# Kernel tuning notes

Hardware: AMD Instinct MI355X
Metric: run time of the kernel (lower is better)

Reference implementation:

```python
import jax, jax.numpy as jnp
import numpy as np

FFT_NORM = 'forward'


def setup_inputs() -> dict:
    key = jax.random.key(0)
    ks = jax.random.split(key, 6)
    B, N, Cin, Cout, T, M = 16, 16384, 64, 64, 256, 2049  # M = modes//2+1 with modes=4096
    x = jax.random.normal(ks[0], (B, N, Cin), dtype=jnp.float32)
    t_emb = jax.random.normal(ks[1], (B, T), dtype=jnp.float32)
    scale = 1.0 / jnp.sqrt(jnp.float32(Cin))
    weights_real = jax.random.normal(ks[2], (M, Cin, Cout), dtype=jnp.float32) * scale
    weights_imag = jax.random.normal(ks[3], (M, Cin, Cout), dtype=jnp.float32) * scale
    dense_real_w = jax.random.normal(ks[4], (M, T), dtype=jnp.float32) * (1.0 / jnp.sqrt(jnp.float32(T)))
    dense_imag_w = jax.random.normal(ks[5], (M, T), dtype=jnp.float32) * (1.0 / jnp.sqrt(jnp.float32(T)))
    return {"x": x, "t_emb": t_emb, "weights_real": weights_real,
            "weights_imag": weights_imag, "dense_real_w": dense_real_w,
            "dense_imag_w": dense_imag_w}


def reference(x, t_emb, weights_real, weights_imag, dense_real_w, dense_imag_w):
    B, N, _ = x.shape
    M, _, Cout = weights_real.shape  # M = modes//2+1
    W = weights_real + 1j * weights_imag  # (M, Cin, Cout) complex64
    # FFT along the grid axis
    x_ft = jnp.fft.rfft(x, axis=-2, norm=FFT_NORM)  # (B, N//2+1, Cin) complex64
    # Time modulation: eqx Linear (bias-free) = t_emb @ W^T
    t_mod = (t_emb @ dense_real_w.T) + 1j * (t_emb @ dense_imag_w.T)  # (B, M)
    # Diagonal modulation + channel mix, exactly equal to the eye/einsum pair:
    # out[b,i,o] = t_mod[b,i] * sum_c x_ft[b,i,c] * W[i,c,o]
    out_trunc = jnp.einsum('bi,bic,ico->bio', t_mod, x_ft[:, :M, :], W)  # (B, M, Cout)
    out_ft = jnp.zeros((B, N // 2 + 1, Cout), dtype=jnp.complex64)
    out_ft = out_ft.at[:, :M, :].set(out_trunc)
    out = jnp.fft.irfft(out_ft, axis=-2, n=N, norm=FFT_NORM)  # (B, N, Cout) float32
    return out
```

## Files before the change

kernel.cpp:

```cpp
#include <hip/hip_runtime.h>
#include <math.h>

#define B_   16
#define N_   16384
#define LOGN 14
#define CIN  64
#define COUT 64
#define T_   256
#define M_   2049

__device__ __forceinline__ unsigned br14(unsigned v) {
  return __brev(v) >> 18;
}

__device__ __forceinline__ int SW(int n) {
  return (n & ~31) | ((n ^ (n >> 5) ^ (n >> 10)) & 31);
}

__device__ __forceinline__ void cmul(float ar, float ai, float br, float bi,
                                     float& rr, float& ri) {
  rr = ar * br - ai * bi;
  ri = ar * bi + ai * br;
}

__device__ __constant__ float C16[16] = {
  1.f, 0.92387953251f, 0.70710678119f, 0.38268343236f, 0.f, -0.38268343236f,
  -0.70710678119f, -0.92387953251f, -1.f, -0.92387953251f, -0.70710678119f,
  -0.38268343236f, 0.f, 0.38268343236f, 0.70710678119f, 0.92387953251f};
__device__ __constant__ float S16[16] = {
  0.f, 0.38268343236f, 0.70710678119f, 0.92387953251f, 1.f, 0.92387953251f,
  0.70710678119f, 0.38268343236f, 0.f, -0.38268343236f, -0.70710678119f,
  -0.92387953251f, -1.f, -0.92387953251f, -0.70710678119f, -0.38268343236f};

template <int SIGN, int S0>
__device__ __forceinline__ void group16(float* __restrict__ sre,
                                        float* __restrict__ sim, int tid) {
  const int lo = tid & ((1 << S0) - 1);
  const int hi = tid >> S0;
  const int base = (hi << (S0 + 4)) + lo;
  int pp[16];
  float xr[16], xi[16];
#pragma unroll
  for (int j = 0; j < 16; ++j) {
    pp[j] = SW(base + (j << S0));
    xr[j] = sre[pp[j]];
    xi[j] = sim[pp[j]];
  }
  float th = 6.283185307179586f * (float)lo / (float)(16 << S0);
  float sn, cs;
  __sincosf(th, &sn, &cs);
  float w1r = cs, w1i = (float)SIGN * sn;
  float w2r, w2i, w4r, w4i, w8r, w8i;
  cmul(w1r, w1i, w1r, w1i, w2r, w2i);
  cmul(w2r, w2i, w2r, w2i, w4r, w4i);
  cmul(w4r, w4i, w4r, w4i, w8r, w8i);
  {
#pragma unroll
    for (int j = 0; j < 16; j += 2) {
      float br, bi;
      cmul(xr[j + 1], xi[j + 1], w8r, w8i, br, bi);
      xr[j + 1] = xr[j] - br; xi[j + 1] = xi[j] - bi;
      xr[j] += br; xi[j] += bi;
    }
  }
  {
    float tr[2], ti[2];
    tr[0] = w4r; ti[0] = w4i;
    cmul(w4r, w4i, C16[4], (float)SIGN * S16[4], tr[1], ti[1]);
#pragma unroll
    for (int j = 0; j < 16; ++j) {
      if ((j & 2) == 0) {
        int jl = j & 1;
        float br, bi;
        cmul(xr[j + 2], xi[j + 2], tr[jl], ti[jl], br, bi);
        xr[j + 2] = xr[j] - br; xi[j + 2] = xi[j] - bi;
        xr[j] += br; xi[j] += bi;
      }
    }
  }
  {
    float tr[4], ti[4];
#pragma unroll
    for (int jl = 0; jl < 4; ++jl)
      cmul(w2r, w2i, C16[2 * jl], (float)SIGN * S16[2 * jl], tr[jl], ti[jl]);
#pragma unroll
    for (int j = 0; j < 16; ++j) {
      if ((j & 4) == 0) {
        int jl = j & 3;
        float br, bi;
        cmul(xr[j + 4], xi[j + 4], tr[jl], ti[jl], br, bi);
        xr[j + 4] = xr[j] - br; xi[j + 4] = xi[j] - bi;
        xr[j] += br; xi[j] += bi;
      }
    }
  }
  {
    float tr[8], ti[8];
#pragma unroll
    for (int jl = 0; jl < 8; ++jl)
      cmul(w1r, w1i, C16[jl], (float)SIGN * S16[jl], tr[jl], ti[jl]);
#pragma unroll
    for (int j = 0; j < 8; ++j) {
      float br, bi;
      cmul(xr[j + 8], xi[j + 8], tr[j], ti[j], br, bi);
      xr[j + 8] = xr[j] - br; xi[j + 8] = xi[j] - bi;
      xr[j] += br; xi[j] += bi;
    }
  }
#pragma unroll
  for (int j = 0; j < 16; ++j) {
    sre[pp[j]] = xr[j];
    sim[pp[j]] = xi[j];
  }
}

template <int SIGN>
__device__ __forceinline__ void stage12(float* __restrict__ sre,
                                        float* __restrict__ sim, int tid) {
  const int lo0 = tid & 511;
  const int gg  = tid >> 9;
  float th = 6.283185307179586f * (float)lo0 / 8192.0f;
  float sn, cs;
  __sincosf(th, &sn, &cs);
  float wtr = cs, wti = (float)SIGN * sn;
#pragma unroll
  for (int s = 0; s < 8; ++s) {
    float twr, twi;
    cmul(wtr, wti, C16[s], (float)SIGN * S16[s], twr, twi);
    int lo = lo0 + 512 * s;
    int i0 = (gg << 13) + lo;
    int p0 = SW(i0), p1 = SW(i0 + 4096);
    float br, bi;
    cmul(sre[p1], sim[p1], twr, twi, br, bi);
    float ar = sre[p0], ai = sim[p0];
    sre[p0] = ar + br; sim[p0] = ai + bi;
    sre[p1] = ar - br; sim[p1] = ai - bi;
  }
}

template <int SIGN>
__device__ __forceinline__ void stage13(float* __restrict__ sre,
                                        float* __restrict__ sim, int tid) {
  float th = 6.283185307179586f * (float)tid / 16384.0f;
  float sn, cs;
  __sincosf(th, &sn, &cs);
  float wtr = cs, wti = (float)SIGN * sn;
#pragma unroll
  for (int s = 0; s < 8; ++s) {
    float twr, twi;
    cmul(wtr, wti, C16[s], (float)SIGN * S16[s], twr, twi);
    int i0 = tid + 1024 * s;
    int p0 = SW(i0), p1 = SW(i0 + 8192);
    float br, bi;
    cmul(sre[p1], sim[p1], twr, twi, br, bi);
    float ar = sre[p0], ai = sim[p0];
    sre[p0] = ar + br; sim[p0] = ai + bi;
    sre[p1] = ar - br; sim[p1] = ai - bi;
  }
}

__device__ __forceinline__ void decode_bc(int id, int& b, int& cp) {
  int q = id >> 6, r = (id >> 3) & 7, p = id & 7;
  int g = q * 8 + p;
  b  = g >> 2;
  cp = (g & 3) * 8 + r;
}

__global__ __launch_bounds__(256) void tmod_kernel(
    const float* __restrict__ t_emb,
    const float* __restrict__ dwr, const float* __restrict__ dwi,
    float* __restrict__ tmr, float* __restrict__ tmi) {
  int wave = threadIdx.x >> 6;
  int lane = threadIdx.x & 63;
  int p = blockIdx.x * 4 + wave;
  if (p >= B_ * M_) return;
  int b = p / M_, i = p % M_;
  float ar = 0.f, ai = 0.f;
  for (int j = 0; j < 4; ++j) {
    int t = lane + 64 * j;
    float te = t_emb[b * T_ + t];
    ar += te * dwr[(size_t)i * T_ + t];
    ai += te * dwi[(size_t)i * T_ + t];
  }
  for (int off = 32; off > 0; off >>= 1) {
    ar += __shfl_down(ar, off, 64);
    ai += __shfl_down(ai, off, 64);
  }
  if (lane == 0) { tmr[b * M_ + i] = ar; tmi[b * M_ + i] = ai; }
}

__global__ __launch_bounds__(1024) void fft_fwd_fused(
    const float* __restrict__ x,
    float* __restrict__ Xre, float* __restrict__ Xim) {
  __shared__ float sre[N_], sim[N_];
  int b, cp;
  decode_bc(blockIdx.x, b, cp);
  const int tid = threadIdx.x;
  const float* xb = x + (size_t)b * N_ * CIN + 2 * cp;
  float2 v[16];
#pragma unroll
  for (int s = 0; s < 16; ++s) {
    int n = tid + 1024 * s;
    v[s] = *(const float2*)(xb + (size_t)n * CIN);
  }
#pragma unroll
  for (int s = 0; s < 16; ++s) {
    int n = tid + 1024 * s;
    int rr = SW((int)br14((unsigned)n));
    sre[rr] = v[s].x;
    sim[rr] = v[s].y;
  }
  __syncthreads();
  group16<-1, 0>(sre, sim, tid); __syncthreads();
  group16<-1, 4>(sre, sim, tid); __syncthreads();
  group16<-1, 8>(sre, sim, tid); __syncthreads();
  stage12<-1>(sre, sim, tid);    __syncthreads();
  stage13<-1>(sre, sim, tid);    __syncthreads();
  const float sc = 1.0f / (float)N_;
  size_t o0 = (size_t)(b * CIN + 2 * cp) * M_;
  size_t o1 = o0 + M_;
  for (int k = tid; k < M_; k += 1024) {
    int mk = (N_ - k) & (N_ - 1);
    int pk = SW(k), pm = SW(mk);
    float zr = sre[pk], zi = sim[pk];
    float mr = sre[pm], mi = sim[pm];
    float X0r = 0.5f * (zr + mr), X0i = 0.5f * (zi - mi);
    float X1r = 0.5f * (zi + mi), X1i = -0.5f * (zr - mr);
    Xre[o0 + k] = X0r * sc; Xim[o0 + k] = X0i * sc;
    Xre[o1 + k] = X1r * sc; Xim[o1 + k] = X1i * sc;
  }
}

__global__ __launch_bounds__(256) void transpose2(
    const float* __restrict__ s0, const float* __restrict__ s1,
    float* __restrict__ d0, float* __restrict__ d1, int R, int C) {
  __shared__ float tile[32][33];
  const float* src = blockIdx.z ? s1 : s0;
  float* dst = blockIdx.z ? d1 : d0;
  int c0 = blockIdx.x * 32, r0 = blockIdx.y * 32;
  int tx = threadIdx.x & 31, ty = threadIdx.x >> 5;
  for (int p = 0; p < 32; p += 8) {
    int r = r0 + ty + p, c = c0 + tx;
    tile[ty + p][tx] = (r < R && c < C) ? src[(size_t)r * C + c] : 0.f;
  }
  __syncthreads();
  for (int p = 0; p < 32; p += 8) {
    int r = c0 + ty + p, c = r0 + tx;
    if (r < C && c < R) dst[(size_t)r * R + c] = tile[tx][ty + p];
  }
}

typedef short  s8v  __attribute__((ext_vector_type(8)));
typedef float  f4v  __attribute__((ext_vector_type(4)));

__device__ __forceinline__ unsigned short f2bf_hi(float x) {
  unsigned u = __float_as_uint(x);
  unsigned r = (u + 0x7fffu + ((u >> 16) & 1u)) >> 16;
  return (unsigned short)r;
}

__device__ __forceinline__ int fbi(int k, int n) {
  return ((((n >> 4) * 2 + (k >> 5)) << 9) | (((n & 15) + (((k >> 3) & 3) << 4)) << 3) | (k & 7));
}
__device__ __forceinline__ int fai(int k, int m) {
  return (((k >> 5) << 9) | (((m & 15) + (((k >> 3) & 3) << 4)) << 3) | (k & 7));
}

__global__ __launch_bounds__(256) void mix_mfma(
    const float* __restrict__ Xtr, const float* __restrict__ Xti,
    const float* __restrict__ Wr_g, const float* __restrict__ Wi_g,
    const float* __restrict__ tmr, const float* __restrict__ tmi,
    float* __restrict__ Yr_g, float* __restrict__ Yi_g) {
  __shared__ __align__(16) unsigned short BrH[4096], BrL[4096], BiH[4096], BiL[4096];
  __shared__ __align__(16) unsigned short ArH[1024], ArL[1024];
  __shared__ __align__(16) unsigned short AiH[1024], AiL[1024];
  __shared__ __align__(16) unsigned short AnH[1024], AnL[1024];
  __shared__ float tms[32];
  const int i   = blockIdx.x;
  const int tid = threadIdx.x;

  const float4* wr4 = (const float4*)(Wr_g + (size_t)i * 4096);
  const float4* wi4 = (const float4*)(Wi_g + (size_t)i * 4096);
#pragma unroll
  for (int it = 0; it < 4; ++it) {
    int f4 = it * 256 + tid;
    float4 vr = wr4[f4];
    float4 vi = wi4[f4];
    int idx0 = f4 * 4;
    float er[4] = {vr.x, vr.y, vr.z, vr.w};
    float ei[4] = {vi.x, vi.y, vi.z, vi.w};
#pragma unroll
    for (int e = 0; e < 4; ++e) {
      int idx = idx0 + e;
      int k = idx >> 6, n = idx & 63;
      int a = fbi(k, n);
      unsigned short h = f2bf_hi(er[e]);
      float hf = __uint_as_float(((unsigned)h) << 16);
      BrH[a] = h; BrL[a] = f2bf_hi(er[e] - hf);
      h = f2bf_hi(ei[e]);
      hf = __uint_as_float(((unsigned)h) << 16);
      BiH[a] = h; BiL[a] = f2bf_hi(ei[e] - hf);
    }
  }
  {
    float4 vr = ((const float4*)(Xtr + (size_t)i * 1024))[tid];
    float4 vi = ((const float4*)(Xti + (size_t)i * 1024))[tid];
    float er[4] = {vr.x, vr.y, vr.z, vr.w};
    float ei[4] = {vi.x, vi.y, vi.z, vi.w};
    int idx0 = tid * 4;
#pragma unroll
    for (int e = 0; e < 4; ++e) {
      int idx = idx0 + e;
      int m = idx >> 6, k = idx & 63;
      int a = fai(k, m);
      unsigned short h = f2bf_hi(er[e]);
      float hf = __uint_as_float(((unsigned)h) << 16);
      ArH[a] = h; ArL[a] = f2bf_hi(er[e] - hf);
      h = f2bf_hi(ei[e]);
      hf = __uint_as_float(((unsigned)h) << 16);
      unsigned short l = f2bf_hi(ei[e] - __uint_as_float(((unsigned)h) << 16));
      AiH[a] = h; AiL[a] = l;
      AnH[a] = h ^ 0x8000u; AnL[a] = l ^ 0x8000u;
    }
  }
  if (tid < 16) {
    tms[tid]      = tmr[tid * M_ + i];
    tms[16 + tid] = tmi[tid * M_ + i];
  }
  __syncthreads();

  const int w = tid >> 6, L = tid & 63;
  const s8v* pArH = (const s8v*)ArH; const s8v* pArL = (const s8v*)ArL;
  const s8v* pAiH = (const s8v*)AiH; const s8v* pAiL = (const s8v*)AiL;
  const s8v* pAnH = (const s8v*)AnH; const s8v* pAnL = (const s8v*)AnL;
  const s8v* pBrH = (const s8v*)BrH; const s8v* pBrL = (const s8v*)BrL;
  const s8v* pBiH = (const s8v*)BiH; const s8v* pBiL = (const s8v*)BiL;

  f4v cr = {0.f, 0.f, 0.f, 0.f}, ci = {0.f, 0.f, 0.f, 0.f};
#pragma unroll
  for (int s = 0; s < 2; ++s) {
    s8v arh = pArH[s * 64 + L], arl = pArL[s * 64 + L];
    s8v aih = pAiH[s * 64 + L], ail = pAiL[s * 64 + L];
    s8v anh = pAnH[s * 64 + L], anl = pAnL[s * 64 + L];
    int bo = (w * 2 + s) * 64 + L;
    s8v brh = pBrH[bo], brl = pBrL[bo];
    s8v bih = pBiH[bo], bil = pBiL[bo];
    cr = __builtin_amdgcn_mfma_f32_16x16x32_bf16(arh, brh, cr, 0, 0, 0);
    cr = __builtin_amdgcn_mfma_f32_16x16x32_bf16(arh, brl, cr, 0, 0, 0);
    cr = __builtin_amdgcn_mfma_f32_16x16x32_bf16(arl, brh, cr, 0, 0, 0);
    cr = __builtin_amdgcn_mfma_f32_16x16x32_bf16(anh, bih, cr, 0, 0, 0);
    cr = __builtin_amdgcn_mfma_f32_16x16x32_bf16(anh, bil, cr, 0, 0, 0);
    cr = __builtin_amdgcn_mfma_f32_16x16x32_bf16(anl, bih, cr, 0, 0, 0);
    ci = __builtin_amdgcn_mfma_f32_16x16x32_bf16(arh, bih, ci, 0, 0, 0);
    ci = __builtin_amdgcn_mfma_f32_16x16x32_bf16(arh, bil, ci, 0, 0, 0);
    ci = __builtin_amdgcn_mfma_f32_16x16x32_bf16(arl, bih, ci, 0, 0, 0);
    ci = __builtin_amdgcn_mfma_f32_16x16x32_bf16(aih, brh, ci, 0, 0, 0);
    ci = __builtin_amdgcn_mfma_f32_16x16x32_bf16(aih, brl, ci, 0, 0, 0);
    ci = __builtin_amdgcn_mfma_f32_16x16x32_bf16(ail, brh, ci, 0, 0, 0);
  }

  const int n = (L & 15) + 16 * w;
  const int quad = L >> 4;
#pragma unroll
  for (int r = 0; r < 4; ++r) {
    int m = quad * 4 + r;
    float tr = tms[m], ti = tms[16 + m];
    float yr = tr * cr[r] - ti * ci[r];
    float yi = tr * ci[r] + ti * cr[r];
    size_t o = (size_t)i * 1024 + m * 64 + n;
    Yr_g[o] = yr;
    Yi_g[o] = yi;
  }
}

__global__ __launch_bounds__(1024) void fft_inv_fused(
    const float* __restrict__ Ytr, const float* __restrict__ Yti,
    float* __restrict__ out) {
  __shared__ float sre[N_], sim[N_];
  int b, cp;
  decode_bc(blockIdx.x, b, cp);
  const int tid = threadIdx.x;
  size_t y0 = (size_t)(b * COUT + 2 * cp) * M_;
  size_t y1 = y0 + M_;
#pragma unroll
  for (int s = 0; s < 16; ++s) {
    int k = tid + 1024 * s;
    float Zr = 0.f, Zi = 0.f;
    if (k < M_) {
      float a0r = Ytr[y0 + k], a0i = Yti[y0 + k];
      float a1r = Ytr[y1 + k], a1i = Yti[y1 + k];
      Zr = a0r - a1i;
      Zi = a0i + a1r;
    }
    int m = N_ - k;
    if (k > 0 && m < M_) {
      float b0r = Ytr[y0 + m], b0i = Yti[y0 + m];
      float b1r = Ytr[y1 + m], b1i = Yti[y1 + m];
      Zr += b0r + b1i;
      Zi += b1r - b0i;
    }
    int rr = SW((int)br14((unsigned)k));
    sre[rr] = Zr;
    sim[rr] = Zi;
  }
  __syncthreads();
  group16<1, 0>(sre, sim, tid); __syncthreads();
  group16<1, 4>(sre, sim, tid); __syncthreads();
  group16<1, 8>(sre, sim, tid); __syncthreads();
  stage12<1>(sre, sim, tid);    __syncthreads();
  stage13<1>(sre, sim, tid);    __syncthreads();
  float* ob = out + (size_t)b * N_ * COUT + 2 * cp;
#pragma unroll
  for (int s = 0; s < 16; ++s) {
    int n = tid + 1024 * s;
    int p = SW(n);
    *(float2*)(ob + (size_t)n * COUT) = make_float2(sre[p], sim[p]);
  }
}

extern "C" void kernel_launch(void* const* d_in, const int* in_sizes, int n_in,
                              void* d_out, int out_size, void* d_ws, size_t ws_size,
                              hipStream_t stream) {
  const float* x    = (const float*)d_in[0];
  const float* temb = (const float*)d_in[1];
  const float* wr   = (const float*)d_in[2];
  const float* wi   = (const float*)d_in[3];
  const float* dwr  = (const float*)d_in[4];
  const float* dwi  = (const float*)d_in[5];
  float* out = (float*)d_out;

  float* ws  = (float*)d_ws;
  float* tmr = ws;
  float* tmi = tmr + 32784;
  float* Xre = tmi + 32784;
  float* Xim = Xre + 2098176;
  float* Xtr = Xim + 2098176;
  float* Xti = Xtr + 2098176;

  tmod_kernel<<<dim3((B_ * M_ + 3) / 4), 256, 0, stream>>>(temb, dwr, dwi, tmr, tmi);
  fft_fwd_fused<<<dim3(B_ * CIN / 2), 1024, 0, stream>>>(x, Xre, Xim);
  transpose2<<<dim3((M_ + 31) / 32, (B_ * CIN + 31) / 32, 2), 256, 0, stream>>>(
      Xre, Xim, Xtr, Xti, B_ * CIN, M_);
  mix_mfma<<<dim3(M_), 256, 0, stream>>>(Xtr, Xti, wr, wi, tmr, tmi, Xtr, Xti);
  transpose2<<<dim3((B_ * COUT + 31) / 32, (M_ + 31) / 32, 2), 256, 0, stream>>>(
      Xtr, Xti, Xre, Xim, M_, B_ * COUT);
  fft_inv_fused<<<dim3(B_ * COUT / 2), 1024, 0, stream>>>(Xre, Xim, out);
}
```

Measured before the change: 330.7 us.

## Process four channels per FFT block with float4 I/O and radix-4 final stages

Each forward and inverse FFT block now handles two packed complex FFTs, four real channels, one after the other. This lets global loads of x and stores of out use float4 instead of float2 and halves the block count. The last two radix-2 stages (stage12 and stage13) are merged into one radix-4 stage, which removes one LDS pass and one barrier per FFT. In exchange each block keeps more values live in registers across the second FFT and runs its two FFTs serially, which lowers parallelism per launch.

```diff
diff --git a/kernel.cpp b/kernel.cpp
--- a/kernel.cpp
+++ b/kernel.cpp
@@ -115,55 +115,52 @@
 }
 
 template <int SIGN>
-__device__ __forceinline__ void stage12(float* __restrict__ sre,
-                                        float* __restrict__ sim, int tid) {
-  const int lo0 = tid & 511;
-  const int gg  = tid >> 9;
-  float th = 6.283185307179586f * (float)lo0 / 8192.0f;
-  float sn, cs;
-  __sincosf(th, &sn, &cs);
-  float wtr = cs, wti = (float)SIGN * sn;
-#pragma unroll
-  for (int s = 0; s < 8; ++s) {
-    float twr, twi;
-    cmul(wtr, wti, C16[s], (float)SIGN * S16[s], twr, twi);
-    int lo = lo0 + 512 * s;
-    int i0 = (gg << 13) + lo;
-    int p0 = SW(i0), p1 = SW(i0 + 4096);
+__device__ __forceinline__ void stage4(float* __restrict__ sre,
+                                       float* __restrict__ sim, int tid) {
+#pragma unroll
+  for (int s = 0; s < 4; ++s) {
+    int i = tid + 1024 * s;
+    int p0 = SW(i), p1 = SW(i + 4096), p2 = SW(i + 8192), p3 = SW(i + 12288);
+    float a0r = sre[p0], a0i = sim[p0];
+    float a1r = sre[p1], a1i = sim[p1];
+    float a2r = sre[p2], a2i = sim[p2];
+    float a3r = sre[p3], a3i = sim[p3];
+    float th = 6.283185307179586f * (float)i / 16384.0f;
+    float sn, cs;
+    __sincosf(th, &sn, &cs);
+    float w1r = cs, w1i = (float)SIGN * sn;
+    float w2r, w2i;
+    cmul(w1r, w1i, w1r, w1i, w2r, w2i);
     float br, bi;
-    cmul(sre[p1], sim[p1], twr, twi, br, bi);
-    float ar = sre[p0], ai = sim[p0];
-    sre[p0] = ar + br; sim[p0] = ai + bi;
-    sre[p1] = ar - br; sim[p1] = ai - bi;
+    cmul(a1r, a1i, w2r, w2i, br, bi);
+    float t0r = a0r + br, t0i = a0i + bi;
+    float t1r = a0r - br, t1i = a0i - bi;
+    cmul(a3r, a3i, w2r, w2i, br, bi);
+    float t2r = a2r + br, t2i = a2i + bi;
+    float t3r = a2r - br, t3i = a2i - bi;
+    cmul(t2r, t2i, w1r, w1i, br, bi);
+    sre[p0] = t0r + br; sim[p0] = t0i + bi;
+    sre[p2] = t0r - br; sim[p2] = t0i - bi;
+    float wbr = -(float)SIGN * w1i, wbi = (float)SIGN * w1r;
+    cmul(t3r, t3i, wbr, wbi, br, bi);
+    sre[p1] = t1r + br; sim[p1] = t1i + bi;
+    sre[p3] = t1r - br; sim[p3] = t1i - bi;
   }
 }
 
 template <int SIGN>
-__device__ __forceinline__ void stage13(float* __restrict__ sre,
-                                        float* __restrict__ sim, int tid) {
-  float th = 6.283185307179586f * (float)tid / 16384.0f;
-  float sn, cs;
-  __sincosf(th, &sn, &cs);
-  float wtr = cs, wti = (float)SIGN * sn;
-#pragma unroll
-  for (int s = 0; s < 8; ++s) {
-    float twr, twi;
-    cmul(wtr, wti, C16[s], (float)SIGN * S16[s], twr, twi);
-    int i0 = tid + 1024 * s;
-    int p0 = SW(i0), p1 = SW(i0 + 8192);
-    float br, bi;
-    cmul(sre[p1], sim[p1], twr, twi, br, bi);
-    float ar = sre[p0], ai = sim[p0];
-    sre[p0] = ar + br; sim[p0] = ai + bi;
-    sre[p1] = ar - br; sim[p1] = ai - bi;
-  }
-}
-
-__device__ __forceinline__ void decode_bc(int id, int& b, int& cp) {
-  int q = id >> 6, r = (id >> 3) & 7, p = id & 7;
-  int g = q * 8 + p;
-  b  = g >> 2;
-  cp = (g & 3) * 8 + r;
+__device__ __forceinline__ void fft_core(float* __restrict__ sre,
+                                         float* __restrict__ sim, int tid) {
+  group16<SIGN, 0>(sre, sim, tid); __syncthreads();
+  group16<SIGN, 4>(sre, sim, tid); __syncthreads();
+  group16<SIGN, 8>(sre, sim, tid); __syncthreads();
+  stage4<SIGN>(sre, sim, tid);     __syncthreads();
+}
+
+__device__ __forceinline__ void decode_bc4(int id, int& b, int& c0) {
+  int t = id >> 6, u = id & 63;
+  b  = u >> 2;
+  c0 = (u & 3) * 16 + t * 4;
 }
 
 __global__ __launch_bounds__(256) void tmod_kernel(
@@ -189,35 +186,12 @@
   if (lane == 0) { tmr[b * M_ + i] = ar; tmi[b * M_ + i] = ai; }
 }
 
-__global__ __launch_bounds__(1024) void fft_fwd_fused(
-    const float* __restrict__ x,
-    float* __restrict__ Xre, float* __restrict__ Xim) {
-  __shared__ float sre[N_], sim[N_];
-  int b, cp;
-  decode_bc(blockIdx.x, b, cp);
-  const int tid = threadIdx.x;
-  const float* xb = x + (size_t)b * N_ * CIN + 2 * cp;
-  float2 v[16];
-#pragma unroll
-  for (int s = 0; s < 16; ++s) {
-    int n = tid + 1024 * s;
-    v[s] = *(const float2*)(xb + (size_t)n * CIN);
-  }
-#pragma unroll
-  for (int s = 0; s < 16; ++s) {
-    int n = tid + 1024 * s;
-    int rr = SW((int)br14((unsigned)n));
-    sre[rr] = v[s].x;
-    sim[rr] = v[s].y;
-  }
-  __syncthreads();
-  group16<-1, 0>(sre, sim, tid); __syncthreads();
-  group16<-1, 4>(sre, sim, tid); __syncthreads();
-  group16<-1, 8>(sre, sim, tid); __syncthreads();
-  stage12<-1>(sre, sim, tid);    __syncthreads();
-  stage13<-1>(sre, sim, tid);    __syncthreads();
+__device__ __forceinline__ void rfft_out(const float* __restrict__ sre,
+                                         const float* __restrict__ sim,
+                                         float* __restrict__ Xre,
+                                         float* __restrict__ Xim,
+                                         size_t o0, int tid) {
   const float sc = 1.0f / (float)N_;
-  size_t o0 = (size_t)(b * CIN + 2 * cp) * M_;
   size_t o1 = o0 + M_;
   for (int k = tid; k < M_; k += 1024) {
     int mk = (N_ - k) & (N_ - 1);
@@ -229,6 +203,45 @@
     Xre[o0 + k] = X0r * sc; Xim[o0 + k] = X0i * sc;
     Xre[o1 + k] = X1r * sc; Xim[o1 + k] = X1i * sc;
   }
+}
+
+__global__ __launch_bounds__(1024) void fft_fwd_fused(
+    const float* __restrict__ x,
+    float* __restrict__ Xre, float* __restrict__ Xim) {
+  __shared__ float sre[N_], sim[N_];
+  int b, c0;
+  decode_bc4(blockIdx.x, b, c0);
+  const int tid = threadIdx.x;
+  const float* xb = x + (size_t)b * N_ * CIN + c0;
+  float4 v[16];
+#pragma unroll
+  for (int s = 0; s < 16; ++s) {
+    int n = tid + 1024 * s;
+    v[s] = *(const float4*)(xb + (size_t)n * CIN);
+  }
+  float2 z2[16];
+#pragma unroll
+  for (int s = 0; s < 16; ++s) {
+    int n = tid + 1024 * s;
+    int rr = SW((int)br14((unsigned)n));
+    sre[rr] = v[s].x;
+    sim[rr] = v[s].y;
+    z2[s] = make_float2(v[s].z, v[s].w);
+  }
+  __syncthreads();
+  fft_core<-1>(sre, sim, tid);
+  rfft_out(sre, sim, Xre, Xim, (size_t)(b * CIN + c0) * M_, tid);
+  __syncthreads();
+#pragma unroll
+  for (int s = 0; s < 16; ++s) {
+    int n = tid + 1024 * s;
+    int rr = SW((int)br14((unsigned)n));
+    sre[rr] = z2[s].x;
+    sim[rr] = z2[s].y;
+  }
+  __syncthreads();
+  fft_core<-1>(sre, sim, tid);
+  rfft_out(sre, sim, Xre, Xim, (size_t)(b * CIN + c0 + 2) * M_, tid);
 }
 
 __global__ __launch_bounds__(256) void transpose2(
@@ -373,14 +386,10 @@
   }
 }
 
-__global__ __launch_bounds__(1024) void fft_inv_fused(
-    const float* __restrict__ Ytr, const float* __restrict__ Yti,
-    float* __restrict__ out) {
-  __shared__ float sre[N_], sim[N_];
-  int b, cp;
-  decode_bc(blockIdx.x, b, cp);
-  const int tid = threadIdx.x;
-  size_t y0 = (size_t)(b * COUT + 2 * cp) * M_;
+__device__ __forceinline__ void herm_load(const float* __restrict__ Ytr,
+                                          const float* __restrict__ Yti,
+                                          size_t y0, float* __restrict__ sre,
+                                          float* __restrict__ sim, int tid) {
   size_t y1 = y0 + M_;
 #pragma unroll
   for (int s = 0; s < 16; ++s) {
@@ -403,18 +412,35 @@
     sre[rr] = Zr;
     sim[rr] = Zi;
   }
-  __syncthreads();
-  group16<1, 0>(sre, sim, tid); __syncthreads();
-  group16<1, 4>(sre, sim, tid); __syncthreads();
-  group16<1, 8>(sre, sim, tid); __syncthreads();
-  stage12<1>(sre, sim, tid);    __syncthreads();
-  stage13<1>(sre, sim, tid);    __syncthreads();
-  float* ob = out + (size_t)b * N_ * COUT + 2 * cp;
+}
+
+__global__ __launch_bounds__(1024) void fft_inv_fused(
+    const float* __restrict__ Ytr, const float* __restrict__ Yti,
+    float* __restrict__ out) {
+  __shared__ float sre[N_], sim[N_];
+  int b, c0;
+  decode_bc4(blockIdx.x, b, c0);
+  const int tid = threadIdx.x;
+  herm_load(Ytr, Yti, (size_t)(b * COUT + c0) * M_, sre, sim, tid);
+  __syncthreads();
+  fft_core<1>(sre, sim, tid);
+  float2 o1[16];
+#pragma unroll
+  for (int s = 0; s < 16; ++s) {
+    int p = SW(tid + 1024 * s);
+    o1[s] = make_float2(sre[p], sim[p]);
+  }
+  __syncthreads();
+  herm_load(Ytr, Yti, (size_t)(b * COUT + c0 + 2) * M_, sre, sim, tid);
+  __syncthreads();
+  fft_core<1>(sre, sim, tid);
+  float* ob = out + (size_t)b * N_ * COUT + c0;
 #pragma unroll
   for (int s = 0; s < 16; ++s) {
     int n = tid + 1024 * s;
     int p = SW(n);
-    *(float2*)(ob + (size_t)n * COUT) = make_float2(sre[p], sim[p]);
+    *(float4*)(ob + (size_t)n * COUT) =
+        make_float4(o1[s].x, o1[s].y, sre[p], sim[p]);
   }
 }
 
@@ -438,11 +464,11 @@
   float* Xti = Xtr + 2098176;
 
   tmod_kernel<<<dim3((B_ * M_ + 3) / 4), 256, 0, stream>>>(temb, dwr, dwi, tmr, tmi);
-  fft_fwd_fused<<<dim3(B_ * CIN / 2), 1024, 0, stream>>>(x, Xre, Xim);
+  fft_fwd_fused<<<dim3(B_ * CIN / 4), 1024, 0, stream>>>(x, Xre, Xim);
   transpose2<<<dim3((M_ + 31) / 32, (B_ * CIN + 31) / 32, 2), 256, 0, stream>>>(
       Xre, Xim, Xtr, Xti, B_ * CIN, M_);
   mix_mfma<<<dim3(M_), 256, 0, stream>>>(Xtr, Xti, wr, wi, tmr, tmi, Xtr, Xti);
   transpose2<<<dim3((B_ * COUT + 31) / 32, (M_ + 31) / 32, 2), 256, 0, stream>>>(
       Xtr, Xti, Xre, Xim, M_, B_ * COUT);
-  fft_inv_fused<<<dim3(B_ * COUT / 2), 1024, 0, stream>>>(Xre, Xim, out);
-}
+  fft_inv_fused<<<dim3(B_ * COUT / 4), 1024, 0, stream>>>(Xre, Xim, out);
+}
```

Result: slower. 556.6 us (+68.3%).
